# Kernel tuning notes

Measured on AMD Instinct MI355X. Metric: run time of the kernel, lower is better.

The kernel has to match this reference:

```python
import jax, jax.numpy as jnp
import numpy as np

# Dimensions per init_kwargs
B, S, D = 2, 2048, 1024          # batch, seq, hidden_size
F = 4096                          # intermediate_size
E, K = 8, 2                       # moe_num_experts, moe_top_k
EPS = 1e-9


def setup_inputs() -> dict:
    key = jax.random.key(0)
    k1, k2, k3, k4 = jax.random.split(key, 4)
    x = jax.random.normal(k1, (B, S, D), dtype=jnp.float32)
    # gate: Linear(D, E, bias=False) -> stored as [D, E] for x @ w_gate
    w_gate = jax.random.normal(k2, (D, E), dtype=jnp.float32) * 0.02
    # per-expert gate_up_proj: Linear(D, 2F, bias=False), stacked over experts -> [E, D, 2F]
    w_gate_up = jax.random.normal(k3, (E, D, 2 * F), dtype=jnp.float32) * 0.02
    # per-expert down_proj: Linear(F, D, bias=False), stacked -> [E, F, D]
    w_down = jax.random.normal(k4, (E, F, D), dtype=jnp.float32) * 0.02
    return {"x": x, "w_gate": w_gate, "w_gate_up": w_gate_up, "w_down": w_down}


def reference(x, w_gate, w_gate_up, w_down):
    # Router
    gate_logits = x @ w_gate                       # [B,S,E]
    gate_probs = jax.nn.softmax(gate_logits, axis=-1)
    # top-k masking + renormalization (top_k < num_experts)
    topk_vals, topk_idx = jax.lax.top_k(gate_probs, K)           # [B,S,K]
    masked = jnp.sum(jax.nn.one_hot(topk_idx, E, dtype=gate_probs.dtype)
                     * topk_vals[..., None], axis=-2)            # [B,S,E]
    denom = jnp.maximum(jnp.sum(masked, axis=-1, keepdims=True), EPS)
    gate_probs = masked / denom

    # Dense per-expert SwiGLU FFN on all tokens (faithful to reference impl)
    gu = jnp.einsum('bsd,edh->ebsh', x, w_gate_up)               # [E,B,S,2F]
    g, u = jnp.split(gu, 2, axis=-1)                             # [E,B,S,F] each
    act = jax.nn.silu(g) * u                                     # [E,B,S,F]
    expert_out = jnp.einsum('ebsf,efd->ebsd', act, w_down)       # [E,B,S,D]

    # Gate-weighted combine
    return jnp.einsum('bse,ebsd->bsd', gate_probs, expert_out)   # [B,S,D]
```

## Files before the change

kernel.cpp:

```cpp
#include <hip/hip_runtime.h>
#include <stdint.h>

#define NTOK 4096
#define DMODEL 1024
#define FF 4096
#define NEXP 8

typedef __bf16 bf16x8 __attribute__((ext_vector_type(8)));
typedef float f32x4 __attribute__((ext_vector_type(4)));
typedef unsigned short u16x8 __attribute__((ext_vector_type(8)));

__device__ __forceinline__ unsigned short f2bf(float f) {
  union { float f; unsigned u; } v; v.f = f;
  unsigned r = v.u + 0x7fffu + ((v.u >> 16) & 1u);
  return (unsigned short)(r >> 16);
}

__global__ __launch_bounds__(256) void k_convert_x(const float4* __restrict__ in,
                                                   ushort4* __restrict__ out, int n4) {
  int stride = gridDim.x * blockDim.x;
  for (int i = blockIdx.x * blockDim.x + threadIdx.x; i < n4; i += stride) {
    float4 v = in[i];
    out[i] = make_ushort4(f2bf(v.x), f2bf(v.y), f2bf(v.z), f2bf(v.w));
  }
}

__global__ __launch_bounds__(256) void k_transpose_bf16(const float* __restrict__ in,
                                                        unsigned short* __restrict__ out,
                                                        int R, int C) {
  __shared__ float tile[64][65];
  const size_t slab = (size_t)R * C;
  const float* ip = in + slab * blockIdx.z;
  unsigned short* op = out + slab * blockIdx.z;
  int c0 = blockIdx.x * 64, r0 = blockIdx.y * 64;
  int tx = threadIdx.x & 15, ty = threadIdx.x >> 4;
#pragma unroll
  for (int i = 0; i < 4; ++i) {
    int r = ty + 16 * i;
    float4 v = *(const float4*)(ip + (size_t)(r0 + r) * C + c0 + tx * 4);
    tile[r][tx * 4 + 0] = v.x;
    tile[r][tx * 4 + 1] = v.y;
    tile[r][tx * 4 + 2] = v.z;
    tile[r][tx * 4 + 3] = v.w;
  }
  __syncthreads();
  int w = threadIdx.x >> 6, lane = threadIdx.x & 63;
  int rc = (lane & 7) * 8;
#pragma unroll
  for (int pass = 0; pass < 2; ++pass) {
    int c = pass * 32 + w * 8 + (lane >> 3);
    u16x8 o;
#pragma unroll
    for (int j = 0; j < 8; ++j) o[j] = f2bf(tile[rc + j][c]);
    *(u16x8*)(op + (size_t)(c0 + c) * R + r0 + rc) = o;
  }
}

__global__ __launch_bounds__(256) void k_router(const float* __restrict__ x,
                                                const float* __restrict__ wg,
                                                int* __restrict__ cnt,
                                                int* __restrict__ elist,
                                                float* __restrict__ gw) {
  int wave = threadIdx.x >> 6, lane = threadIdx.x & 63;
  int t = blockIdx.x * 4 + wave;
  const float* xp = x + (size_t)t * DMODEL;
  float a[8] = {0, 0, 0, 0, 0, 0, 0, 0};
#pragma unroll
  for (int i = 0; i < DMODEL / 64; ++i) {
    int d = lane + 64 * i;
    float xv = xp[d];
    float4 w0 = *(const float4*)(wg + d * 8);
    float4 w1 = *(const float4*)(wg + d * 8 + 4);
    a[0] += xv * w0.x; a[1] += xv * w0.y; a[2] += xv * w0.z; a[3] += xv * w0.w;
    a[4] += xv * w1.x; a[5] += xv * w1.y; a[6] += xv * w1.z; a[7] += xv * w1.w;
  }
#pragma unroll
  for (int off = 32; off > 0; off >>= 1)
#pragma unroll
    for (int e = 0; e < 8; ++e) a[e] += __shfl_down(a[e], off, 64);
  if (lane == 0) {
    int e0 = 0;
    for (int e = 1; e < 8; ++e) if (a[e] > a[e0]) e0 = e;
    int e1 = (e0 == 0) ? 1 : 0;
    for (int e = 0; e < 8; ++e) if (e != e0 && a[e] > a[e1]) e1 = e;
    float p = __expf(a[e1] - a[e0]);
    float inv = 1.0f / (1.0f + p);
    int p0 = atomicAdd(&cnt[e0], 1);
    elist[e0 * NTOK + p0] = 2 * t;
    gw[2 * t] = inv;
    int p1 = atomicAdd(&cnt[e1], 1);
    elist[e1 * NTOK + p1] = 2 * t + 1;
    gw[2 * t + 1] = p * inv;
  }
}

__global__ __launch_bounds__(512, 2) void k_gemm1(const unsigned short* __restrict__ xb,
                                                  const unsigned short* __restrict__ wgu,
                                                  const int* __restrict__ cnt,
                                                  const int* __restrict__ elist,
                                                  unsigned short* __restrict__ act)
{
  __shared__ __align__(16) unsigned short sA[2][256 * 64];
  __shared__ __align__(16) unsigned short sB[2][256 * 64];

  const int e = blockIdx.z;
  const int n_e = cnt[e];
  const int m0 = blockIdx.y * 256;
  if (m0 >= n_e) return;
  const int c0 = blockIdx.x * 128;
  const int tid = threadIdx.x;
  const int w = tid >> 6, lane = tid & 63;
  const int wr = w >> 2, wc = w & 3;
  const int* el = elist + e * NTOK;
  const int csub = ((lane & 7) ^ (lane >> 3)) * 8;
  const int srow = w * 8 + (lane >> 3);

  int tokrow[4];
  size_t baddr[4];
  const unsigned short* wb = wgu + (size_t)e * (2 * FF) * DMODEL;
#pragma unroll
  for (int i = 0; i < 4; ++i) {
    int r = i * 64 + srow;
    int idx = m0 + r;
    tokrow[i] = el[idx < n_e ? idx : 0] >> 1;
    int strip = r >> 6, off = r & 63;
    int wrow = (off < 32) ? (c0 + strip * 32 + off) : (FF + c0 + strip * 32 + off - 32);
    baddr[i] = (size_t)wrow * DMODEL;
  }

  f32x4 acc[8][4];
  f32x4 zero = {0.f, 0.f, 0.f, 0.f};
#pragma unroll
  for (int m = 0; m < 8; ++m)
#pragma unroll
    for (int n = 0; n < 4; ++n) acc[m][n] = zero;

  auto stage = [&](int buf, int k0) {
#pragma unroll
    for (int i = 0; i < 4; ++i) {
      const unsigned short* g2 = xb + (size_t)tokrow[i] * DMODEL + k0 + csub;
      __builtin_amdgcn_global_load_lds((const __attribute__((address_space(1))) void*)g2,
                                       (__attribute__((address_space(3))) void*)(&sA[buf][(i * 64 + w * 8) * 64]),
                                       16, 0, 0);
    }
#pragma unroll
    for (int i = 0; i < 4; ++i) {
      const unsigned short* g2 = wb + baddr[i] + k0 + csub;
      __builtin_amdgcn_global_load_lds((const __attribute__((address_space(1))) void*)g2,
                                       (__attribute__((address_space(3))) void*)(&sB[buf][(i * 64 + w * 8) * 64]),
                                       16, 0, 0);
    }
  };

  auto compute = [&](int buf) {
#pragma unroll
    for (int kk = 0; kk < 2; ++kk) {
      const int xk = ((kk * 4 + (lane >> 4)) ^ (lane & 7)) * 8;
      bf16x8 af[8], bf[4];
#pragma unroll
      for (int m = 0; m < 8; ++m)
        af[m] = *(const bf16x8*)(&sA[buf][(wr * 128 + m * 16 + (lane & 15)) * 64 + xk]);
#pragma unroll
      for (int n = 0; n < 4; ++n)
        bf[n] = *(const bf16x8*)(&sB[buf][(wc * 64 + n * 16 + (lane & 15)) * 64 + xk]);
#pragma unroll
      for (int m = 0; m < 8; ++m)
#pragma unroll
        for (int n = 0; n < 4; ++n)
          acc[m][n] = __builtin_amdgcn_mfma_f32_16x16x32_bf16(af[m], bf[n], acc[m][n], 0, 0, 0);
    }
  };

  stage(0, 0);
  __syncthreads();
  int cur = 0;
  for (int t = 0; t < DMODEL / 64; ++t) {
    if (t + 1 < DMODEL / 64) stage(cur ^ 1, (t + 1) * 64);
    compute(cur);
    __syncthreads();
    cur ^= 1;
  }

#pragma unroll
  for (int m = 0; m < 8; ++m) {
#pragma unroll
    for (int r = 0; r < 4; ++r) {
      int idx = m0 + wr * 128 + m * 16 + (lane >> 4) * 4 + r;
      if (idx < n_e) {
        int p = el[idx];
        unsigned short* ap = act + (size_t)p * FF + c0 + wc * 32;
#pragma unroll
        for (int n = 0; n < 2; ++n) {
          float gv = acc[m][n][r];
          float u = acc[m][n + 2][r];
          float s = gv / (1.0f + __expf(-gv));
          ap[n * 16 + (lane & 15)] = f2bf(s * u);
        }
      }
    }
  }
}

__global__ __launch_bounds__(256, 4) void k_gemm2(const unsigned short* __restrict__ actb,
                                                  const unsigned short* __restrict__ wd,
                                                  const int* __restrict__ cnt,
                                                  const int* __restrict__ elist,
                                                  const float* __restrict__ gw,
                                                  float* __restrict__ out_slot)
{
  __shared__ __align__(16) unsigned short sA[128 * 64];
  __shared__ __align__(16) unsigned short sB[128 * 64];

  const int bid = blockIdx.x;
  const int orig = (bid & 7) * 256 + (bid >> 3);
  const int g = orig >> 5;
  const int y = orig & 31;
  const int e = g >> 3;
  const int n_e = cnt[e];
  const int m0 = y * 128;
  if (m0 >= n_e) return;
  const int n0 = (g & 7) * 128;
  const int tid = threadIdx.x;
  const int w = tid >> 6, lane = tid & 63;
  const int wr = w >> 1, wc = w & 1;
  const int* el = elist + e * NTOK;
  const int csub = ((lane & 7) ^ (lane >> 3)) * 8;

  int prow[4];
  size_t baddr[4];
  const unsigned short* wb = wd + (size_t)e * DMODEL * FF;
#pragma unroll
  for (int i = 0; i < 4; ++i) {
    int r = i * 32 + w * 8 + (lane >> 3);
    int idx = m0 + r;
    prow[i] = el[idx < n_e ? idx : 0];
    baddr[i] = (size_t)(n0 + r) * FF;
  }

  f32x4 acc[4][4];
  f32x4 zero = {0.f, 0.f, 0.f, 0.f};
#pragma unroll
  for (int m = 0; m < 4; ++m)
#pragma unroll
    for (int n = 0; n < 4; ++n) acc[m][n] = zero;

  for (int k0 = 0; k0 < FF; k0 += 64) {
#pragma unroll
    for (int i = 0; i < 4; ++i) {
      const unsigned short* g2 = actb + (size_t)prow[i] * FF + k0 + csub;
      __builtin_amdgcn_global_load_lds((const __attribute__((address_space(1))) void*)g2,
                                       (__attribute__((address_space(3))) void*)(&sA[(i * 32 + w * 8) * 64]),
                                       16, 0, 0);
    }
#pragma unroll
    for (int i = 0; i < 4; ++i) {
      const unsigned short* g2 = wb + baddr[i] + k0 + csub;
      __builtin_amdgcn_global_load_lds((const __attribute__((address_space(1))) void*)g2,
                                       (__attribute__((address_space(3))) void*)(&sB[(i * 32 + w * 8) * 64]),
                                       16, 0, 0);
    }
    __syncthreads();
#pragma unroll
    for (int kk = 0; kk < 2; ++kk) {
      const int xk = ((kk * 4 + (lane >> 4)) ^ (lane & 7)) * 8;
      bf16x8 af[4], bf[4];
#pragma unroll
      for (int m = 0; m < 4; ++m)
        af[m] = *(const bf16x8*)(&sA[(wr * 64 + m * 16 + (lane & 15)) * 64 + xk]);
#pragma unroll
      for (int n = 0; n < 4; ++n)
        bf[n] = *(const bf16x8*)(&sB[(wc * 64 + n * 16 + (lane & 15)) * 64 + xk]);
#pragma unroll
      for (int m = 0; m < 4; ++m)
#pragma unroll
        for (int n = 0; n < 4; ++n)
          acc[m][n] = __builtin_amdgcn_mfma_f32_16x16x32_bf16(af[m], bf[n], acc[m][n], 0, 0, 0);
    }
    __syncthreads();
  }

#pragma unroll
  for (int m = 0; m < 4; ++m) {
#pragma unroll
    for (int r = 0; r < 4; ++r) {
      int idx = m0 + wr * 64 + m * 16 + (lane >> 4) * 4 + r;
      if (idx < n_e) {
        int p = el[idx];
        float wgt = gw[p];
        float* op = out_slot + (size_t)p * DMODEL + n0 + wc * 64;
#pragma unroll
        for (int n = 0; n < 4; ++n)
          op[n * 16 + (lane & 15)] = acc[m][n][r] * wgt;
      }
    }
  }
}

__global__ __launch_bounds__(256) void k_combine(const float4* __restrict__ slot,
                                                 float4* __restrict__ out, int n4) {
  int stride = gridDim.x * blockDim.x;
  for (int i = blockIdx.x * blockDim.x + threadIdx.x; i < n4; i += stride) {
    int t = i >> 8;
    int j = i & 255;
    float4 a = slot[(size_t)(2 * t) * 256 + j];
    float4 b = slot[(size_t)(2 * t + 1) * 256 + j];
    float4 o;
    o.x = a.x + b.x; o.y = a.y + b.y; o.z = a.z + b.z; o.w = a.w + b.w;
    out[i] = o;
  }
}

extern "C" void kernel_launch(void* const* d_in, const int* in_sizes, int n_in,
                              void* d_out, int out_size, void* d_ws, size_t ws_size,
                              hipStream_t stream) {
  const float* x   = (const float*)d_in[0];
  const float* wg  = (const float*)d_in[1];
  const float* wgu = (const float*)d_in[2];
  const float* wd  = (const float*)d_in[3];
  float* out = (float*)d_out;

  char* ws = (char*)d_ws;
  size_t off = 0;
  auto alloc = [&](size_t bytes) -> char* {
    char* p = ws + off;
    off += (bytes + 255) & ~(size_t)255;
    return p;
  };
  unsigned short* wgu_t = (unsigned short*)alloc((size_t)NEXP * 2 * FF * DMODEL * 2);
  unsigned short* wd_t  = (unsigned short*)alloc((size_t)NEXP * DMODEL * FF * 2);
  unsigned short* actb  = (unsigned short*)alloc((size_t)2 * NTOK * FF * 2);
  float* out_slot       = (float*)alloc((size_t)2 * NTOK * DMODEL * 4);
  unsigned short* xb    = (unsigned short*)alloc((size_t)NTOK * DMODEL * 2);
  int* elist            = (int*)alloc((size_t)NEXP * NTOK * 4);
  float* gw             = (float*)alloc((size_t)2 * NTOK * 4);
  int* cnt              = (int*)alloc(256);
  if (off > ws_size) return;

  hipMemsetAsync(cnt, 0, 256, stream);
  k_convert_x<<<1024, 256, 0, stream>>>((const float4*)x, (ushort4*)xb, NTOK * DMODEL / 4);
  k_transpose_bf16<<<dim3(2 * FF / 64, DMODEL / 64, NEXP), 256, 0, stream>>>(wgu, wgu_t, DMODEL, 2 * FF);
  k_transpose_bf16<<<dim3(DMODEL / 64, FF / 64, NEXP), 256, 0, stream>>>(wd, wd_t, FF, DMODEL);
  k_router<<<NTOK / 4, 256, 0, stream>>>(x, wg, cnt, elist, gw);
  k_gemm1<<<dim3(FF / 128, NTOK / 256, NEXP), 512, 0, stream>>>(xb, wgu_t, cnt, elist, actb);
  k_gemm2<<<2048, 256, 0, stream>>>(actb, wd_t, cnt, elist, gw, out_slot);
  k_combine<<<2048, 256, 0, stream>>>((const float4*)out_slot, (float4*)out, NTOK * DMODEL / 4);
}
```

Baseline: 564.8 us.

## Widen gemm2 tiles to 128x256 and fuse combine via atomic adds

The down-projection GEMM now uses 512-thread blocks with a 128x256 output tile, so each activation tile is reused across twice as many output columns. The separate combine kernel and its per-slot fp32 buffer are removed. Each block instead atomically adds its gate-weighted results into the zeroed output, which saves a full write and re-read of the slot buffer and one kernel launch. In exchange it adds an output memset, atomic traffic, and a nondeterministic summation order.

After: 565.1 us. About the same (+0.1%).

```diff
diff --git a/kernel.cpp b/kernel.cpp
--- a/kernel.cpp
+++ b/kernel.cpp
@@ -201,41 +201,43 @@
   }
 }
 
-__global__ __launch_bounds__(256, 4) void k_gemm2(const unsigned short* __restrict__ actb,
+__global__ __launch_bounds__(512, 2) void k_gemm2(const unsigned short* __restrict__ actb,
                                                   const unsigned short* __restrict__ wd,
                                                   const int* __restrict__ cnt,
                                                   const int* __restrict__ elist,
                                                   const float* __restrict__ gw,
-                                                  float* __restrict__ out_slot)
+                                                  float* __restrict__ out)
 {
   __shared__ __align__(16) unsigned short sA[128 * 64];
-  __shared__ __align__(16) unsigned short sB[128 * 64];
+  __shared__ __align__(16) unsigned short sB[256 * 64];
 
   const int bid = blockIdx.x;
-  const int orig = (bid & 7) * 256 + (bid >> 3);
+  const int orig = (bid & 7) * 128 + (bid >> 3);
   const int g = orig >> 5;
   const int y = orig & 31;
-  const int e = g >> 3;
+  const int e = g >> 2;
   const int n_e = cnt[e];
   const int m0 = y * 128;
   if (m0 >= n_e) return;
-  const int n0 = (g & 7) * 128;
+  const int n0 = (g & 3) * 256;
   const int tid = threadIdx.x;
   const int w = tid >> 6, lane = tid & 63;
-  const int wr = w >> 1, wc = w & 1;
+  const int wr = w >> 2, wc = w & 3;
   const int* el = elist + e * NTOK;
   const int csub = ((lane & 7) ^ (lane >> 3)) * 8;
-
-  int prow[4];
+  const int srow = w * 8 + (lane >> 3);
+
+  int prow[2];
   size_t baddr[4];
   const unsigned short* wb = wd + (size_t)e * DMODEL * FF;
 #pragma unroll
-  for (int i = 0; i < 4; ++i) {
-    int r = i * 32 + w * 8 + (lane >> 3);
-    int idx = m0 + r;
+  for (int i = 0; i < 2; ++i) {
+    int idx = m0 + i * 64 + srow;
     prow[i] = el[idx < n_e ? idx : 0];
-    baddr[i] = (size_t)(n0 + r) * FF;
-  }
+  }
+#pragma unroll
+  for (int j = 0; j < 4; ++j)
+    baddr[j] = (size_t)(n0 + j * 64 + srow) * FF;
 
   f32x4 acc[4][4];
   f32x4 zero = {0.f, 0.f, 0.f, 0.f};
@@ -246,17 +248,17 @@
 
   for (int k0 = 0; k0 < FF; k0 += 64) {
 #pragma unroll
-    for (int i = 0; i < 4; ++i) {
+    for (int i = 0; i < 2; ++i) {
       const unsigned short* g2 = actb + (size_t)prow[i] * FF + k0 + csub;
       __builtin_amdgcn_global_load_lds((const __attribute__((address_space(1))) void*)g2,
-                                       (__attribute__((address_space(3))) void*)(&sA[(i * 32 + w * 8) * 64]),
+                                       (__attribute__((address_space(3))) void*)(&sA[(i * 64 + w * 8) * 64]),
                                        16, 0, 0);
     }
 #pragma unroll
-    for (int i = 0; i < 4; ++i) {
-      const unsigned short* g2 = wb + baddr[i] + k0 + csub;
+    for (int j = 0; j < 4; ++j) {
+      const unsigned short* g2 = wb + baddr[j] + k0 + csub;
       __builtin_amdgcn_global_load_lds((const __attribute__((address_space(1))) void*)g2,
-                                       (__attribute__((address_space(3))) void*)(&sB[(i * 32 + w * 8) * 64]),
+                                       (__attribute__((address_space(3))) void*)(&sB[(j * 64 + w * 8) * 64]),
                                        16, 0, 0);
     }
     __syncthreads();
@@ -287,26 +289,12 @@
       if (idx < n_e) {
         int p = el[idx];
         float wgt = gw[p];
-        float* op = out_slot + (size_t)p * DMODEL + n0 + wc * 64;
+        float* op = out + (size_t)(p >> 1) * DMODEL + n0 + wc * 64;
 #pragma unroll
         for (int n = 0; n < 4; ++n)
-          op[n * 16 + (lane & 15)] = acc[m][n][r] * wgt;
+          atomicAdd(&op[n * 16 + (lane & 15)], acc[m][n][r] * wgt);
       }
     }
-  }
-}
-
-__global__ __launch_bounds__(256) void k_combine(const float4* __restrict__ slot,
-                                                 float4* __restrict__ out, int n4) {
-  int stride = gridDim.x * blockDim.x;
-  for (int i = blockIdx.x * blockDim.x + threadIdx.x; i < n4; i += stride) {
-    int t = i >> 8;
-    int j = i & 255;
-    float4 a = slot[(size_t)(2 * t) * 256 + j];
-    float4 b = slot[(size_t)(2 * t + 1) * 256 + j];
-    float4 o;
-    o.x = a.x + b.x; o.y = a.y + b.y; o.z = a.z + b.z; o.w = a.w + b.w;
-    out[i] = o;
   }
 }
 
@@ -329,7 +317,6 @@
   unsigned short* wgu_t = (unsigned short*)alloc((size_t)NEXP * 2 * FF * DMODEL * 2);
   unsigned short* wd_t  = (unsigned short*)alloc((size_t)NEXP * DMODEL * FF * 2);
   unsigned short* actb  = (unsigned short*)alloc((size_t)2 * NTOK * FF * 2);
-  float* out_slot       = (float*)alloc((size_t)2 * NTOK * DMODEL * 4);
   unsigned short* xb    = (unsigned short*)alloc((size_t)NTOK * DMODEL * 2);
   int* elist            = (int*)alloc((size_t)NEXP * NTOK * 4);
   float* gw             = (float*)alloc((size_t)2 * NTOK * 4);
@@ -337,11 +324,11 @@
   if (off > ws_size) return;
 
   hipMemsetAsync(cnt, 0, 256, stream);
+  hipMemsetAsync(out, 0, (size_t)NTOK * DMODEL * 4, stream);
   k_convert_x<<<1024, 256, 0, stream>>>((const float4*)x, (ushort4*)xb, NTOK * DMODEL / 4);
   k_transpose_bf16<<<dim3(2 * FF / 64, DMODEL / 64, NEXP), 256, 0, stream>>>(wgu, wgu_t, DMODEL, 2 * FF);
   k_transpose_bf16<<<dim3(DMODEL / 64, FF / 64, NEXP), 256, 0, stream>>>(wd, wd_t, FF, DMODEL);
   k_router<<<NTOK / 4, 256, 0, stream>>>(x, wg, cnt, elist, gw);
   k_gemm1<<<dim3(FF / 128, NTOK / 256, NEXP), 512, 0, stream>>>(xb, wgu_t, cnt, elist, actb);
-  k_gemm2<<<2048, 256, 0, stream>>>(actb, wd_t, cnt, elist, gw, out_slot);
-  k_combine<<<2048, 256, 0, stream>>>((const float4*)out_slot, (float4*)out, NTOK * DMODEL / 4);
-}
+  k_gemm2<<<1024, 512, 0, stream>>>(actb, wd_t, cnt, elist, gw, out);
+}
```
